# Kernel tuning notes

Measured on AMD Instinct MI355X. Metric: run time of the kernel, lower is better.

## Reference

```python
import jax, jax.numpy as jnp
import numpy as np

N_NODES = 100000
N_EDGES = 800000
H = 128
MAX_Z = 1000
N_GRAPHS = 500  # batch = repeat(arange(500), 200); subgraphs are contiguous


def setup_inputs() -> dict:
    key = jax.random.key(0)
    ks = jax.random.split(key, 16)
    z = jax.random.randint(ks[0], (N_NODES,), 0, MAX_Z)
    edge_index = jax.random.randint(ks[1], (2, N_EDGES), 0, N_NODES)
    batch = jnp.repeat(jnp.arange(N_GRAPHS), N_NODES // N_GRAPHS)
    edge_mask = jax.random.randint(ks[2], (N_EDGES,), 0, 2).astype(bool)
    s = 1.0 / np.sqrt(H)
    inp = {
        "z": z, "edge_index": edge_index, "batch": batch, "edge_mask": edge_mask,
        "z_table": jax.random.normal(ks[3], (MAX_Z, H), dtype=jnp.float32) * 0.02,
        "W0": jax.random.uniform(ks[4], (H, H), minval=-s, maxval=s),
        "b0": jax.random.uniform(ks[5], (H,), minval=-s, maxval=s),
        "W1": jax.random.uniform(ks[6], (H, H), minval=-s, maxval=s),
        "b1": jax.random.uniform(ks[7], (H,), minval=-s, maxval=s),
        "W2": jax.random.uniform(ks[8], (H, H), minval=-s, maxval=s),
        "b2": jax.random.uniform(ks[9], (H,), minval=-s, maxval=s),
        "lin1_w": jax.random.uniform(ks[10], (H, H), minval=-s, maxval=s),
        "lin1_b": jax.random.uniform(ks[11], (H,), minval=-s, maxval=s),
        "lin2_w": jax.random.uniform(ks[12], (H, 1), minval=-s, maxval=s),
        "lin2_b": jax.random.uniform(ks[13], (1,), minval=-s, maxval=s),
    }
    return inp


def _gcn_conv(x, W, b, src, dst, w):
    # PyG GCNConv with self-loops (fill=1) and symmetric normalization.
    xw = x @ W                                                # [N,H]
    deg = jax.ops.segment_sum(w, dst, num_segments=N_NODES) + 1.0
    dinv = jax.lax.rsqrt(deg)                                 # deg >= 1 (self-loop)
    coef = (dinv[src] * w * dinv[dst])[:, None]               # [E,1]
    out = jax.ops.segment_sum(coef * xw[src], dst, num_segments=N_NODES)
    out = out + (dinv * dinv)[:, None] * xw                   # self-loop messages
    return out + b


def reference(z, edge_index, batch, edge_mask, z_table,
              W0, b0, W1, b1, W2, b2, lin1_w, lin1_b, lin2_w, lin2_b):
    x = z_table[z]                                            # z embedding, [N,H]
    src, dst = edge_index[0], edge_index[1]
    # fuse='minus': edge_index[:, edge_mask] == zero-weight masked-out edges
    w = edge_mask.astype(x.dtype)
    x = jax.nn.relu(_gcn_conv(x, W0, b0, src, dst, w))        # dropout: eval mode
    x = jax.nn.relu(_gcn_conv(x, W1, b1, src, dst, w))
    x = _gcn_conv(x, W2, b2, src, dst, w)
    # hadamard pooling: first two nodes of each (sorted, contiguous) subgraph
    center = jnp.searchsorted(batch, jnp.arange(N_GRAPHS))
    x = x[center] * x[center + 1]                             # [G,H]
    x = jax.nn.relu(x @ lin1_w + lin1_b)
    return x @ lin2_w + lin2_b                                # [G,1]
```

## Files before the change

kernel.cpp:

```cpp
#include <hip/hip_runtime.h>

#define N_NODES 100000
#define N_EDGES 800000
#define H 128
#define N_GRAPHS 500
#define ELL_CAP 32
#define EB 782
#define NB 391
#define MAXC1 33008
#define NC_ROWS 1008

typedef __attribute__((ext_vector_type(8))) short bf16x8;
typedef __attribute__((ext_vector_type(4))) float f32x4;

__device__ __forceinline__ unsigned short f2bf(float f) {
    union { float f; unsigned u; } x; x.f = f;
    unsigned r = x.u + 0x7fffu + ((x.u >> 16) & 1u);
    return (unsigned short)(r >> 16);
}
__device__ __forceinline__ float bf2f(unsigned short u) {
    return __uint_as_float((unsigned)u << 16);
}
__device__ __forceinline__ bool is_center(int v) { return (v % 200) < 2; }

__global__ void k_init(int* cnt, int* fill, unsigned char* f0, unsigned char* f1,
                       int* ctrs) {
    int i = blockIdx.x * 256 + threadIdx.x;
    if (i < N_NODES) {
        cnt[i] = 0; fill[i] = 0;
        unsigned char c = is_center(i) ? 1 : 0;
        f0[i] = c; f1[i] = c;
    }
    if (i < 2) ctrs[i] = 0;
}

__global__ void k_scan1(const int4* src4, const int4* dst4, const int4* mask4,
                        int* cnt, unsigned char* f1) {
    int i = blockIdx.x * 256 + threadIdx.x;
    if (i >= N_EDGES / 4) return;
    int4 s = src4[i], d = dst4[i], mk = mask4[i];
    if (mk.x) { atomicAdd(&cnt[d.x], 1); if (is_center(d.x)) f1[s.x] = 1; }
    if (mk.y) { atomicAdd(&cnt[d.y], 1); if (is_center(d.y)) f1[s.y] = 1; }
    if (mk.z) { atomicAdd(&cnt[d.z], 1); if (is_center(d.z)) f1[s.z] = 1; }
    if (mk.w) { atomicAdd(&cnt[d.w], 1); if (is_center(d.w)) f1[s.w] = 1; }
}

__global__ void k_flag0(const int4* src4, const int4* dst4, const int4* mask4,
                        const unsigned char* f1, unsigned char* f0) {
    int i = blockIdx.x * 256 + threadIdx.x;
    if (i >= N_EDGES / 4) return;
    int4 s = src4[i], d = dst4[i], mk = mask4[i];
    if (mk.x && f1[d.x]) f0[s.x] = 1;
    if (mk.y && f1[d.y]) f0[s.y] = 1;
    if (mk.z && f1[d.z]) f0[s.z] = 1;
    if (mk.w && f1[d.w]) f0[s.w] = 1;
}

__global__ void k_fillcompact(const int4* src4, const int4* dst4, const int4* mask4,
                              const int* cnt, const unsigned char* f0,
                              const unsigned char* f1, int* fill, int2* pairs,
                              int* list0, int* list1, int* ctrs) {
    int b = blockIdx.x;
    if (b < EB) {
        int i = b * 256 + threadIdx.x;
        if (i >= N_EDGES / 4) return;
        int4 s4 = src4[i], d4 = dst4[i], mk = mask4[i];
        int ss[4] = { s4.x, s4.y, s4.z, s4.w };
        int dd[4] = { d4.x, d4.y, d4.z, d4.w };
        int mm[4] = { mk.x, mk.y, mk.z, mk.w };
#pragma unroll
        for (int q = 0; q < 4; q++) {
            if (!mm[q]) continue;
            int d = dd[q];
            if (f0[d] | f1[d]) {
                int s = ss[q];
                int p = atomicAdd(&fill[d], 1);
                if (p < ELL_CAP) {
                    float coef = rsqrtf(1.0f + (float)cnt[s]) *
                                 rsqrtf(1.0f + (float)cnt[d]);
                    pairs[(size_t)d * ELL_CAP + p] = make_int2(s, __float_as_int(coef));
                }
            }
        }
    } else {
        int v = (b - EB) * 256 + threadIdx.x;
        if (v >= N_NODES) return;
        unsigned char a1 = f1[v];
        unsigned char a0 = f0[v] | a1;
        if (a0) { int i = atomicAdd(&ctrs[0], 1); list0[i] = v; }
        if (a1) { int j = atomicAdd(&ctrs[1], 1); list1[j] = v; }
    }
}

__global__ void k_packw(const float* W0, const float* W1, const float* W2,
                        unsigned short* Wp) {
    int wi = blockIdx.x >> 3;
    const float* W = (wi == 0) ? W0 : (wi == 1) ? W1 : W2;
    int t = (blockIdx.x & 7) * 256 + threadIdx.x;
    int lane = t & 63, kt = (t >> 6) & 3, c = t >> 8;
    int quad = lane >> 4, n = c * 16 + (lane & 15);
    unsigned short o[8];
#pragma unroll
    for (int j = 0; j < 8; j++)
        o[j] = f2bf(W[(kt * 32 + quad * 8 + j) * H + n]);
    ushort4 lo = { o[0], o[1], o[2], o[3] }, hi = { o[4], o[5], o[6], o[7] };
    unsigned short* dst = Wp + (size_t)wi * 16384 + (size_t)t * 8;
    *(ushort4*)(dst)     = lo;
    *(ushort4*)(dst + 4) = hi;
}

__global__ __launch_bounds__(256) void k_layerA(const int* z, const float* tab,
                                                const int2* pairs, const int* cnt,
                                                const int* list, const int* countp,
                                                const unsigned short* Wp,
                                                const float* bias,
                                                unsigned short* xb) {
    __shared__ unsigned short yt[16][136];
    int count = *countp;
    int t = blockIdx.x;
    if (t * 16 >= count) return;
    int tid = threadIdx.x, lane = tid & 63, wv = tid >> 6;
    int l2 = lane * 2;

    for (int q = 0; q < 4; q++) {
        int r = t * 16 + wv * 4 + q;
        float ax = 0.f, ay = 0.f;
        if (r < count) {
            int v = list[r];
            int n = cnt[v]; if (n > ELL_CAP) n = ELL_CAP;
            const int2* pr = pairs + (size_t)v * ELL_CAP;
            int2 myp = (lane < n) ? pr[lane] : make_int2(0, 0);
            int px = myp.x; float pc = __int_as_float(myp.y);
            float dv = rsqrtf(1.0f + (float)n);
            float sc = dv * dv;
            float2 xs = *(const float2*)(tab + (size_t)z[v] * H + l2);
            ax = sc * xs.x; ay = sc * xs.y;
            int k = 0;
            for (; k + 3 < n; k += 4) {
                int s0 = __shfl(px, k),   s1 = __shfl(px, k + 1);
                int s2 = __shfl(px, k + 2), s3 = __shfl(px, k + 3);
                float c0 = __shfl(pc, k),   c1 = __shfl(pc, k + 1);
                float c2 = __shfl(pc, k + 2), c3 = __shfl(pc, k + 3);
                int z0 = z[s0], z1 = z[s1], z2 = z[s2], z3 = z[s3];
                float2 m0 = *(const float2*)(tab + (size_t)z0 * H + l2);
                float2 m1 = *(const float2*)(tab + (size_t)z1 * H + l2);
                float2 m2 = *(const float2*)(tab + (size_t)z2 * H + l2);
                float2 m3 = *(const float2*)(tab + (size_t)z3 * H + l2);
                ax += c0 * m0.x + c1 * m1.x + c2 * m2.x + c3 * m3.x;
                ay += c0 * m0.y + c1 * m1.y + c2 * m2.y + c3 * m3.y;
            }
            for (; k < n; k++) {
                int s = __shfl(px, k); float c = __shfl(pc, k);
                float2 m = *(const float2*)(tab + (size_t)z[s] * H + l2);
                ax += c * m.x; ay += c * m.y;
            }
        }
        ushort2 o; o.x = f2bf(ax); o.y = f2bf(ay);
        *(ushort2*)&yt[wv * 4 + q][l2] = o;
    }
    __syncthreads();

    int m = lane & 15, quad = lane >> 4;
    bf16x8 a0 = *(const bf16x8*)&yt[m][quad * 8];
    bf16x8 a1 = *(const bf16x8*)&yt[m][32 + quad * 8];
    bf16x8 a2 = *(const bf16x8*)&yt[m][64 + quad * 8];
    bf16x8 a3 = *(const bf16x8*)&yt[m][96 + quad * 8];

    f32x4 acc[2];
#pragma unroll
    for (int c2 = 0; c2 < 2; c2++) {
        int c = wv * 2 + c2;
        const unsigned short* bp = Wp + ((size_t)(c * 4) * 64 + lane) * 8;
        bf16x8 b0 = *(const bf16x8*)(bp);
        bf16x8 b1 = *(const bf16x8*)(bp + 64 * 8);
        bf16x8 b2 = *(const bf16x8*)(bp + 128 * 8);
        bf16x8 b3 = *(const bf16x8*)(bp + 192 * 8);
        f32x4 a = (f32x4){0.f, 0.f, 0.f, 0.f};
        a = __builtin_amdgcn_mfma_f32_16x16x32_bf16(a0, b0, a, 0, 0, 0);
        a = __builtin_amdgcn_mfma_f32_16x16x32_bf16(a1, b1, a, 0, 0, 0);
        a = __builtin_amdgcn_mfma_f32_16x16x32_bf16(a2, b2, a, 0, 0, 0);
        a = __builtin_amdgcn_mfma_f32_16x16x32_bf16(a3, b3, a, 0, 0, 0);
        acc[c2] = a;
    }

    int r0 = t * 16 + quad * 4;
    int rid[4];
#pragma unroll
    for (int i = 0; i < 4; i++) {
        int r = r0 + i;
        rid[i] = (r < count) ? list[r] : -1;
    }
#pragma unroll
    for (int c2 = 0; c2 < 2; c2++) {
        int col = (wv * 2 + c2) * 16 + m;
        float bv = bias[col];
#pragma unroll
        for (int i = 0; i < 4; i++)
            if (rid[i] >= 0)
                xb[(size_t)rid[i] * H + col] = f2bf(fmaxf(acc[c2][i] + bv, 0.f));
    }
}

__global__ __launch_bounds__(256) void k_layerB(const unsigned short* xin,
                                                const int2* pairs, const int* cnt,
                                                const int* list, const int* countp,
                                                const unsigned short* Wp,
                                                const float* bias,
                                                unsigned short* xb) {
    __shared__ unsigned short yt[16][136];
    int count = *countp;
    int t = blockIdx.x;
    if (t * 16 >= count) return;
    int tid = threadIdx.x, lane = tid & 63, wv = tid >> 6;
    int l2 = lane * 2;

    for (int q = 0; q < 4; q++) {
        int r = t * 16 + wv * 4 + q;
        float ax = 0.f, ay = 0.f;
        if (r < count) {
            int v = list[r];
            int n = cnt[v]; if (n > ELL_CAP) n = ELL_CAP;
            const int2* pr = pairs + (size_t)v * ELL_CAP;
            int2 myp = (lane < n) ? pr[lane] : make_int2(0, 0);
            int px = myp.x; float pc = __int_as_float(myp.y);
            float dv = rsqrtf(1.0f + (float)n);
            float sc = dv * dv;
            ushort2 xs = *(const ushort2*)(xin + (size_t)v * H + l2);
            ax = sc * bf2f(xs.x); ay = sc * bf2f(xs.y);
            int k = 0;
            for (; k + 3 < n; k += 4) {
                int s0 = __shfl(px, k),   s1 = __shfl(px, k + 1);
                int s2 = __shfl(px, k + 2), s3 = __shfl(px, k + 3);
                float c0 = __shfl(pc, k),   c1 = __shfl(pc, k + 1);
                float c2 = __shfl(pc, k + 2), c3 = __shfl(pc, k + 3);
                ushort2 m0 = *(const ushort2*)(xin + (size_t)s0 * H + l2);
                ushort2 m1 = *(const ushort2*)(xin + (size_t)s1 * H + l2);
                ushort2 m2 = *(const ushort2*)(xin + (size_t)s2 * H + l2);
                ushort2 m3 = *(const ushort2*)(xin + (size_t)s3 * H + l2);
                ax += c0 * bf2f(m0.x) + c1 * bf2f(m1.x) + c2 * bf2f(m2.x) + c3 * bf2f(m3.x);
                ay += c0 * bf2f(m0.y) + c1 * bf2f(m1.y) + c2 * bf2f(m2.y) + c3 * bf2f(m3.y);
            }
            for (; k < n; k++) {
                int s = __shfl(px, k); float c = __shfl(pc, k);
                ushort2 m = *(const ushort2*)(xin + (size_t)s * H + l2);
                ax += c * bf2f(m.x); ay += c * bf2f(m.y);
            }
        }
        ushort2 o; o.x = f2bf(ax); o.y = f2bf(ay);
        *(ushort2*)&yt[wv * 4 + q][l2] = o;
    }
    __syncthreads();

    int m = lane & 15, quad = lane >> 4;
    bf16x8 a0 = *(const bf16x8*)&yt[m][quad * 8];
    bf16x8 a1 = *(const bf16x8*)&yt[m][32 + quad * 8];
    bf16x8 a2 = *(const bf16x8*)&yt[m][64 + quad * 8];
    bf16x8 a3 = *(const bf16x8*)&yt[m][96 + quad * 8];

    f32x4 acc[2];
#pragma unroll
    for (int c2 = 0; c2 < 2; c2++) {
        int c = wv * 2 + c2;
        const unsigned short* bp = Wp + ((size_t)(c * 4) * 64 + lane) * 8;
        bf16x8 b0 = *(const bf16x8*)(bp);
        bf16x8 b1 = *(const bf16x8*)(bp + 64 * 8);
        bf16x8 b2 = *(const bf16x8*)(bp + 128 * 8);
        bf16x8 b3 = *(const bf16x8*)(bp + 192 * 8);
        f32x4 a = (f32x4){0.f, 0.f, 0.f, 0.f};
        a = __builtin_amdgcn_mfma_f32_16x16x32_bf16(a0, b0, a, 0, 0, 0);
        a = __builtin_amdgcn_mfma_f32_16x16x32_bf16(a1, b1, a, 0, 0, 0);
        a = __builtin_amdgcn_mfma_f32_16x16x32_bf16(a2, b2, a, 0, 0, 0);
        a = __builtin_amdgcn_mfma_f32_16x16x32_bf16(a3, b3, a, 0, 0, 0);
        acc[c2] = a;
    }

    int r0 = t * 16 + quad * 4;
    int rid[4];
#pragma unroll
    for (int i = 0; i < 4; i++) {
        int r = r0 + i;
        rid[i] = (r < count) ? list[r] : -1;
    }
#pragma unroll
    for (int c2 = 0; c2 < 2; c2++) {
        int col = (wv * 2 + c2) * 16 + m;
        float bv = bias[col];
#pragma unroll
        for (int i = 0; i < 4; i++)
            if (rid[i] >= 0)
                xb[(size_t)rid[i] * H + col] = f2bf(fmaxf(acc[c2][i] + bv, 0.f));
    }
}

__global__ __launch_bounds__(256) void k_layer2(const unsigned short* xin,
                                                const int2* pairs, const int* cnt,
                                                const unsigned short* Wp,
                                                const float* b2,
                                                const float* l1w, const float* l1b,
                                                const float* l2w, const float* l2b,
                                                float* out) {
    __shared__ unsigned short yt[16][136];
    __shared__ float ct[16][132];
    int t = blockIdx.x;
    int tid = threadIdx.x, lane = tid & 63, wv = tid >> 6;
    int l2 = lane * 2;

    for (int q = 0; q < 4; q++) {
        int idx = t * 16 + wv * 4 + q;
        float ax = 0.f, ay = 0.f;
        if (idx < 2 * N_GRAPHS) {
            int v = (idx >> 1) * 200 + (idx & 1);
            int n = cnt[v]; if (n > ELL_CAP) n = ELL_CAP;
            const int2* pr = pairs + (size_t)v * ELL_CAP;
            int2 myp = (lane < n) ? pr[lane] : make_int2(0, 0);
            int px = myp.x; float pc = __int_as_float(myp.y);
            float dv = rsqrtf(1.0f + (float)n);
            float sc = dv * dv;
            ushort2 xs = *(const ushort2*)(xin + (size_t)v * H + l2);
            ax = sc * bf2f(xs.x); ay = sc * bf2f(xs.y);
            for (int k = 0; k < n; k++) {
                int s = __shfl(px, k); float c = __shfl(pc, k);
                ushort2 m = *(const ushort2*)(xin + (size_t)s * H + l2);
                ax += c * bf2f(m.x); ay += c * bf2f(m.y);
            }
        }
        ushort2 o; o.x = f2bf(ax); o.y = f2bf(ay);
        *(ushort2*)&yt[wv * 4 + q][l2] = o;
    }
    __syncthreads();

    int m = lane & 15, quad = lane >> 4;
    bf16x8 a0 = *(const bf16x8*)&yt[m][quad * 8];
    bf16x8 a1 = *(const bf16x8*)&yt[m][32 + quad * 8];
    bf16x8 a2 = *(const bf16x8*)&yt[m][64 + quad * 8];
    bf16x8 a3 = *(const bf16x8*)&yt[m][96 + quad * 8];

#pragma unroll
    for (int c2 = 0; c2 < 2; c2++) {
        int c = wv * 2 + c2;
        const unsigned short* bp = Wp + ((size_t)(c * 4) * 64 + lane) * 8;
        bf16x8 b0 = *(const bf16x8*)(bp);
        bf16x8 b1 = *(const bf16x8*)(bp + 64 * 8);
        bf16x8 bb = *(const bf16x8*)(bp + 128 * 8);
        bf16x8 b3 = *(const bf16x8*)(bp + 192 * 8);
        f32x4 a = (f32x4){0.f, 0.f, 0.f, 0.f};
        a = __builtin_amdgcn_mfma_f32_16x16x32_bf16(a0, b0, a, 0, 0, 0);
        a = __builtin_amdgcn_mfma_f32_16x16x32_bf16(a1, b1, a, 0, 0, 0);
        a = __builtin_amdgcn_mfma_f32_16x16x32_bf16(a2, bb, a, 0, 0, 0);
        a = __builtin_amdgcn_mfma_f32_16x16x32_bf16(a3, b3, a, 0, 0, 0);
        int col = c * 16 + m;
        float bv = b2[col];
#pragma unroll
        for (int i = 0; i < 4; i++)
            ct[quad * 4 + i][col] = a[i] + bv;
    }
    __syncthreads();

    int gl = tid >> 5, jq = tid & 31, j4 = jq * 4;
    int g = t * 8 + gl;
    float4 h = *(const float4*)(l1b + j4);
    const float* r0 = &ct[2 * gl][0];
    const float* r1 = &ct[2 * gl + 1][0];
#pragma unroll 4
    for (int k = 0; k < H; k++) {
        float pk = r0[k] * r1[k];
        float4 wv4 = *(const float4*)(l1w + (size_t)k * H + j4);
        h.x += pk * wv4.x; h.y += pk * wv4.y;
        h.z += pk * wv4.z; h.w += pk * wv4.w;
    }
    float4 l2v = *(const float4*)(l2w + j4);
    float s = fmaxf(h.x, 0.f) * l2v.x + fmaxf(h.y, 0.f) * l2v.y +
              fmaxf(h.z, 0.f) * l2v.z + fmaxf(h.w, 0.f) * l2v.w;
#pragma unroll
    for (int d = 16; d > 0; d >>= 1) s += __shfl_xor(s, d, 32);
    if (jq == 0 && g < N_GRAPHS) out[g] = s + l2b[0];
}

extern "C" void kernel_launch(void* const* d_in, const int* in_sizes, int n_in,
                              void* d_out, int out_size, void* d_ws, size_t ws_size,
                              hipStream_t stream) {
    const int*   z    = (const int*)d_in[0];
    const int*   esrc = (const int*)d_in[1];
    const int*   edst = ((const int*)d_in[1]) + N_EDGES;
    const int*   mask = (const int*)d_in[3];
    const float* ztab = (const float*)d_in[4];
    const float* W0   = (const float*)d_in[5];
    const float* b0   = (const float*)d_in[6];
    const float* W1   = (const float*)d_in[7];
    const float* b1   = (const float*)d_in[8];
    const float* W2   = (const float*)d_in[9];
    const float* b2   = (const float*)d_in[10];
    const float* l1w  = (const float*)d_in[11];
    const float* l1b  = (const float*)d_in[12];
    const float* l2w  = (const float*)d_in[13];
    const float* l2b  = (const float*)d_in[14];
    float* out = (float*)d_out;

    char* w = (char*)d_ws;
    size_t o = 0;
    auto carve = [&](size_t bytes) { char* p = w + o; o = (o + bytes + 255) & ~(size_t)255; return p; };
    unsigned short* xb    = (unsigned short*)carve((size_t)N_NODES * H * 2);
    int*            cnt   = (int*)carve((size_t)N_NODES * 4);
    int*            fill  = (int*)carve((size_t)N_NODES * 4);
    int2*           pairs = (int2*)carve((size_t)N_NODES * ELL_CAP * 8);
    unsigned char*  f0    = (unsigned char*)carve(N_NODES);
    unsigned char*  f1    = (unsigned char*)carve(N_NODES);
    int*            list0 = (int*)carve((size_t)N_NODES * 4);
    int*            list1 = (int*)carve((size_t)N_NODES * 4);
    int*            ctrs  = (int*)carve(256);
    unsigned short* Wp    = (unsigned short*)carve((size_t)3 * 16384 * 2);

    const int4* src4  = (const int4*)esrc;
    const int4* dst4  = (const int4*)edst;
    const int4* mask4 = (const int4*)mask;

    k_init       <<<NB, 256, 0, stream>>>(cnt, fill, f0, f1, ctrs);
    k_packw      <<<24, 256, 0, stream>>>(W0, W1, W2, Wp);
    k_scan1      <<<EB, 256, 0, stream>>>(src4, dst4, mask4, cnt, f1);
    k_flag0      <<<EB, 256, 0, stream>>>(src4, dst4, mask4, f1, f0);
    k_fillcompact<<<EB + NB, 256, 0, stream>>>(src4, dst4, mask4, cnt, f0, f1,
                                               fill, pairs, list0, list1, ctrs);

    k_layerA<<<(N_NODES + 15) / 16, 256, 0, stream>>>(z, ztab, pairs, cnt, list0,
                                                      &ctrs[0], Wp, b0, xb);
    k_layerB<<<MAXC1 / 16, 256, 0, stream>>>(xb, pairs, cnt, list1, &ctrs[1],
                                             Wp + 16384, b1, xb);
    k_layer2<<<NC_ROWS / 16, 256, 0, stream>>>(xb, pairs, cnt, Wp + 32768, b2,
                                               l1w, l1b, l2w, l2b, out);
}
```

Baseline: 200.6 us.

## Build full ELL once and derive receptive-field lists by traversing from centers

Replaces the three full edge passes (degree count, flag propagation, filtered fill) with one pass that builds an int-only ELL adjacency for all nodes. The 1-hop and 2-hop receptive sets are then found by walking the adjacency outward from the 1000 center nodes, using atomicExch flags to deduplicate and append to the lists. Per-edge normalization coefficients are no longer stored; each layer recomputes them from fill counts. This removes two passes over the edge arrays and halves the ELL storage. In exchange it writes ELL rows for every node, and the layers do extra gathers of fill[src].

```diff
diff --git a/kernel.cpp b/kernel.cpp
--- a/kernel.cpp
+++ b/kernel.cpp
@@ -5,7 +5,6 @@
 #define H 128
 #define N_GRAPHS 500
 #define ELL_CAP 32
-#define EB 782
 #define NB 391
 #define MAXC1 33008
 #define NC_ROWS 1008
@@ -21,74 +20,51 @@
 __device__ __forceinline__ float bf2f(unsigned short u) {
     return __uint_as_float((unsigned)u << 16);
 }
-__device__ __forceinline__ bool is_center(int v) { return (v % 200) < 2; }
-
-__global__ void k_init(int* cnt, int* fill, unsigned char* f0, unsigned char* f1,
-                       int* ctrs) {
+
+__global__ void k_init(int* fill, int* f0, int* f1, int* ctrs) {
     int i = blockIdx.x * 256 + threadIdx.x;
-    if (i < N_NODES) {
-        cnt[i] = 0; fill[i] = 0;
-        unsigned char c = is_center(i) ? 1 : 0;
-        f0[i] = c; f1[i] = c;
-    }
+    if (i < N_NODES) { fill[i] = 0; f0[i] = 0; f1[i] = 0; }
     if (i < 2) ctrs[i] = 0;
 }
 
-__global__ void k_scan1(const int4* src4, const int4* dst4, const int4* mask4,
-                        int* cnt, unsigned char* f1) {
-    int i = blockIdx.x * 256 + threadIdx.x;
-    if (i >= N_EDGES / 4) return;
-    int4 s = src4[i], d = dst4[i], mk = mask4[i];
-    if (mk.x) { atomicAdd(&cnt[d.x], 1); if (is_center(d.x)) f1[s.x] = 1; }
-    if (mk.y) { atomicAdd(&cnt[d.y], 1); if (is_center(d.y)) f1[s.y] = 1; }
-    if (mk.z) { atomicAdd(&cnt[d.z], 1); if (is_center(d.z)) f1[s.z] = 1; }
-    if (mk.w) { atomicAdd(&cnt[d.w], 1); if (is_center(d.w)) f1[s.w] = 1; }
-}
-
-__global__ void k_flag0(const int4* src4, const int4* dst4, const int4* mask4,
-                        const unsigned char* f1, unsigned char* f0) {
-    int i = blockIdx.x * 256 + threadIdx.x;
-    if (i >= N_EDGES / 4) return;
-    int4 s = src4[i], d = dst4[i], mk = mask4[i];
-    if (mk.x && f1[d.x]) f0[s.x] = 1;
-    if (mk.y && f1[d.y]) f0[s.y] = 1;
-    if (mk.z && f1[d.z]) f0[s.z] = 1;
-    if (mk.w && f1[d.w]) f0[s.w] = 1;
-}
-
-__global__ void k_fillcompact(const int4* src4, const int4* dst4, const int4* mask4,
-                              const int* cnt, const unsigned char* f0,
-                              const unsigned char* f1, int* fill, int2* pairs,
-                              int* list0, int* list1, int* ctrs) {
-    int b = blockIdx.x;
-    if (b < EB) {
-        int i = b * 256 + threadIdx.x;
-        if (i >= N_EDGES / 4) return;
-        int4 s4 = src4[i], d4 = dst4[i], mk = mask4[i];
-        int ss[4] = { s4.x, s4.y, s4.z, s4.w };
-        int dd[4] = { d4.x, d4.y, d4.z, d4.w };
-        int mm[4] = { mk.x, mk.y, mk.z, mk.w };
-#pragma unroll
-        for (int q = 0; q < 4; q++) {
-            if (!mm[q]) continue;
-            int d = dd[q];
-            if (f0[d] | f1[d]) {
-                int s = ss[q];
-                int p = atomicAdd(&fill[d], 1);
-                if (p < ELL_CAP) {
-                    float coef = rsqrtf(1.0f + (float)cnt[s]) *
-                                 rsqrtf(1.0f + (float)cnt[d]);
-                    pairs[(size_t)d * ELL_CAP + p] = make_int2(s, __float_as_int(coef));
-                }
-            }
+__global__ void k_edge(const int* src, const int* dst, const int* mask,
+                       int* fill, int* ell) {
+    int e = blockIdx.x * 256 + threadIdx.x;
+    if (e >= N_EDGES) return;
+    if (!mask[e]) return;
+    int d = dst[e];
+    int p = atomicAdd(&fill[d], 1);
+    if (p < ELL_CAP) ell[(size_t)d * ELL_CAP + p] = src[e];
+}
+
+__global__ void k_n1(const int* fill, const int* ell, int* f1, int* f0,
+                     int* list1, int* list0, int* ctrs) {
+    int lane = threadIdx.x & 63, wv = threadIdx.x >> 6;
+    int c = blockIdx.x * 4 + wv;
+    if (c >= 2 * N_GRAPHS) return;
+    int v = (c >> 1) * 200 + (c & 1);
+    int n = fill[v]; if (n > ELL_CAP) n = ELL_CAP;
+    int s = (lane < n) ? ell[(size_t)v * ELL_CAP + lane] : ((lane == n) ? v : -1);
+    if (s >= 0) {
+        if (atomicExch(&f1[s], 1) == 0) {
+            list1[atomicAdd(&ctrs[1], 1)] = s;
+            if (atomicExch(&f0[s], 1) == 0)
+                list0[atomicAdd(&ctrs[0], 1)] = s;
         }
-    } else {
-        int v = (b - EB) * 256 + threadIdx.x;
-        if (v >= N_NODES) return;
-        unsigned char a1 = f1[v];
-        unsigned char a0 = f0[v] | a1;
-        if (a0) { int i = atomicAdd(&ctrs[0], 1); list0[i] = v; }
-        if (a1) { int j = atomicAdd(&ctrs[1], 1); list1[j] = v; }
+    }
+}
+
+__global__ void k_n0(const int* fill, const int* ell, const int* list1,
+                     int* f0, int* list0, int* ctrs) {
+    int lane = threadIdx.x & 63, wv = threadIdx.x >> 6;
+    int i = blockIdx.x * 4 + wv;
+    if (i >= ctrs[1]) return;
+    int v = list1[i];
+    int n = fill[v]; if (n > ELL_CAP) n = ELL_CAP;
+    if (lane < n) {
+        int s = ell[(size_t)v * ELL_CAP + lane];
+        if (atomicExch(&f0[s], 1) == 0)
+            list0[atomicAdd(&ctrs[0], 1)] = s;
     }
 }
 
@@ -110,7 +86,7 @@
 }
 
 __global__ __launch_bounds__(256) void k_layerA(const int* z, const float* tab,
-                                                const int2* pairs, const int* cnt,
+                                                const int* ell, const int* fill,
                                                 const int* list, const int* countp,
                                                 const unsigned short* Wp,
                                                 const float* bias,
@@ -127,11 +103,12 @@
         float ax = 0.f, ay = 0.f;
         if (r < count) {
             int v = list[r];
-            int n = cnt[v]; if (n > ELL_CAP) n = ELL_CAP;
-            const int2* pr = pairs + (size_t)v * ELL_CAP;
-            int2 myp = (lane < n) ? pr[lane] : make_int2(0, 0);
-            int px = myp.x; float pc = __int_as_float(myp.y);
-            float dv = rsqrtf(1.0f + (float)n);
+            int ntrue = fill[v];
+            int n = ntrue > ELL_CAP ? ELL_CAP : ntrue;
+            float dv = rsqrtf(1.0f + (float)ntrue);
+            int px = (lane < n) ? ell[(size_t)v * ELL_CAP + lane] : 0;
+            float pc = 0.f;
+            if (lane < n) pc = rsqrtf(1.0f + (float)fill[px]) * dv;
             float sc = dv * dv;
             float2 xs = *(const float2*)(tab + (size_t)z[v] * H + l2);
             ax = sc * xs.x; ay = sc * xs.y;
@@ -202,7 +179,7 @@
 }
 
 __global__ __launch_bounds__(256) void k_layerB(const unsigned short* xin,
-                                                const int2* pairs, const int* cnt,
+                                                const int* ell, const int* fill,
                                                 const int* list, const int* countp,
                                                 const unsigned short* Wp,
                                                 const float* bias,
@@ -219,11 +196,12 @@
         float ax = 0.f, ay = 0.f;
         if (r < count) {
             int v = list[r];
-            int n = cnt[v]; if (n > ELL_CAP) n = ELL_CAP;
-            const int2* pr = pairs + (size_t)v * ELL_CAP;
-            int2 myp = (lane < n) ? pr[lane] : make_int2(0, 0);
-            int px = myp.x; float pc = __int_as_float(myp.y);
-            float dv = rsqrtf(1.0f + (float)n);
+            int ntrue = fill[v];
+            int n = ntrue > ELL_CAP ? ELL_CAP : ntrue;
+            float dv = rsqrtf(1.0f + (float)ntrue);
+            int px = (lane < n) ? ell[(size_t)v * ELL_CAP + lane] : 0;
+            float pc = 0.f;
+            if (lane < n) pc = rsqrtf(1.0f + (float)fill[px]) * dv;
             float sc = dv * dv;
             ushort2 xs = *(const ushort2*)(xin + (size_t)v * H + l2);
             ax = sc * bf2f(xs.x); ay = sc * bf2f(xs.y);
@@ -293,7 +271,7 @@
 }
 
 __global__ __launch_bounds__(256) void k_layer2(const unsigned short* xin,
-                                                const int2* pairs, const int* cnt,
+                                                const int* ell, const int* fill,
                                                 const unsigned short* Wp,
                                                 const float* b2,
                                                 const float* l1w, const float* l1b,
@@ -310,11 +288,12 @@
         float ax = 0.f, ay = 0.f;
         if (idx < 2 * N_GRAPHS) {
             int v = (idx >> 1) * 200 + (idx & 1);
-            int n = cnt[v]; if (n > ELL_CAP) n = ELL_CAP;
-            const int2* pr = pairs + (size_t)v * ELL_CAP;
-            int2 myp = (lane < n) ? pr[lane] : make_int2(0, 0);
-            int px = myp.x; float pc = __int_as_float(myp.y);
-            float dv = rsqrtf(1.0f + (float)n);
+            int ntrue = fill[v];
+            int n = ntrue > ELL_CAP ? ELL_CAP : ntrue;
+            float dv = rsqrtf(1.0f + (float)ntrue);
+            int px = (lane < n) ? ell[(size_t)v * ELL_CAP + lane] : 0;
+            float pc = 0.f;
+            if (lane < n) pc = rsqrtf(1.0f + (float)fill[px]) * dv;
             float sc = dv * dv;
             ushort2 xs = *(const ushort2*)(xin + (size_t)v * H + l2);
             ax = sc * bf2f(xs.x); ay = sc * bf2f(xs.y);
@@ -400,31 +379,25 @@
     size_t o = 0;
     auto carve = [&](size_t bytes) { char* p = w + o; o = (o + bytes + 255) & ~(size_t)255; return p; };
     unsigned short* xb    = (unsigned short*)carve((size_t)N_NODES * H * 2);
-    int*            cnt   = (int*)carve((size_t)N_NODES * 4);
     int*            fill  = (int*)carve((size_t)N_NODES * 4);
-    int2*           pairs = (int2*)carve((size_t)N_NODES * ELL_CAP * 8);
-    unsigned char*  f0    = (unsigned char*)carve(N_NODES);
-    unsigned char*  f1    = (unsigned char*)carve(N_NODES);
+    int*            ell   = (int*)carve((size_t)N_NODES * ELL_CAP * 4);
+    int*            f0    = (int*)carve((size_t)N_NODES * 4);
+    int*            f1    = (int*)carve((size_t)N_NODES * 4);
     int*            list0 = (int*)carve((size_t)N_NODES * 4);
-    int*            list1 = (int*)carve((size_t)N_NODES * 4);
+    int*            list1 = (int*)carve((size_t)MAXC1 * 4);
     int*            ctrs  = (int*)carve(256);
     unsigned short* Wp    = (unsigned short*)carve((size_t)3 * 16384 * 2);
 
-    const int4* src4  = (const int4*)esrc;
-    const int4* dst4  = (const int4*)edst;
-    const int4* mask4 = (const int4*)mask;
-
-    k_init       <<<NB, 256, 0, stream>>>(cnt, fill, f0, f1, ctrs);
-    k_packw      <<<24, 256, 0, stream>>>(W0, W1, W2, Wp);
-    k_scan1      <<<EB, 256, 0, stream>>>(src4, dst4, mask4, cnt, f1);
-    k_flag0      <<<EB, 256, 0, stream>>>(src4, dst4, mask4, f1, f0);
-    k_fillcompact<<<EB + NB, 256, 0, stream>>>(src4, dst4, mask4, cnt, f0, f1,
-                                               fill, pairs, list0, list1, ctrs);
-
-    k_layerA<<<(N_NODES + 15) / 16, 256, 0, stream>>>(z, ztab, pairs, cnt, list0,
+    k_init <<<NB, 256, 0, stream>>>(fill, f0, f1, ctrs);
+    k_packw<<<24, 256, 0, stream>>>(W0, W1, W2, Wp);
+    k_edge <<<(N_EDGES + 255) / 256, 256, 0, stream>>>(esrc, edst, mask, fill, ell);
+    k_n1   <<<(2 * N_GRAPHS + 3) / 4, 256, 0, stream>>>(fill, ell, f1, f0, list1, list0, ctrs);
+    k_n0   <<<(MAXC1 + 3) / 4, 256, 0, stream>>>(fill, ell, list1, f0, list0, ctrs);
+
+    k_layerA<<<(N_NODES + 15) / 16, 256, 0, stream>>>(z, ztab, ell, fill, list0,
                                                       &ctrs[0], Wp, b0, xb);
-    k_layerB<<<MAXC1 / 16, 256, 0, stream>>>(xb, pairs, cnt, list1, &ctrs[1],
+    k_layerB<<<MAXC1 / 16, 256, 0, stream>>>(xb, ell, fill, list1, &ctrs[1],
                                              Wp + 16384, b1, xb);
-    k_layer2<<<NC_ROWS / 16, 256, 0, stream>>>(xb, pairs, cnt, Wp + 32768, b2,
+    k_layer2<<<NC_ROWS / 16, 256, 0, stream>>>(xb, ell, fill, Wp + 32768, b2,
                                                l1w, l1b, l2w, l2b, out);
 }
```

Result: slower. 232.8 us (+16.0%).
